# Performance work log

Measured on AMD Instinct MI355X. Metric: run time of the kernel, lower is better.

Reference implementation:

```python
import jax, jax.numpy as jnp
import numpy as np

H = 150
PASSES = 5
NSETS = 2
N = 50000
E = 400000
G = 64
SLOPE = 0.01  # torch leaky_relu default


def setup_inputs() -> dict:
    key = jax.random.key(0)
    ks = jax.random.split(key, 20)
    def u(k, shape, fan):
        lim = 1.0 / np.sqrt(fan)
        return jax.random.uniform(k, shape, jnp.float32, -lim, lim)
    return {
        "nodes": jax.random.normal(ks[0], (N, H), jnp.float32),
        "problem_type": jax.random.uniform(ks[1], (G, 1), jnp.float32),
        "edge_W": u(ks[2], (NSETS, H, H), H),
        "edge_b": u(ks[3], (NSETS, H), H),
        "gru_w_ih": u(ks[4], (3 * H, H), H),
        "gru_w_hh": u(ks[5], (3 * H, H), H),
        "gru_b_ih": u(ks[6], (3 * H,), H),
        "gru_b_hh": u(ks[7], (3 * H,), H),
        "fc1_w": u(ks[8], (80, 151), 151),
        "fc1_b": u(ks[9], (80,), 151),
        "fc2_w": u(ks[10], (80, 80), 80),
        "fc2_b": u(ks[11], (80,), 80),
        "fcL_w": u(ks[12], (10, 80), 80),
        "fcL_b": u(ks[13], (10,), 80),
        "edges": jax.random.randint(ks[14], (NSETS, E, 2), 0, N),
        "graph_ids": jnp.sort(jax.random.randint(ks[15], (N,), 0, G)),
        "tbptt": 0,
    }


def _gru_cell(x, h, w_ih, w_hh, b_ih, b_hh):
    gi = x @ w_ih.T + b_ih  # [N, 3H]
    gh = h @ w_hh.T + b_hh
    ir, iz, inn = jnp.split(gi, 3, axis=-1)
    hr, hz, hn = jnp.split(gh, 3, axis=-1)
    r = jax.nn.sigmoid(ir + hr)
    z = jax.nn.sigmoid(iz + hz)
    n = jnp.tanh(inn + r * hn)
    return (1.0 - z) * n + z * h


def reference(nodes, problem_type, edge_W, edge_b, gru_w_ih, gru_w_hh,
              gru_b_ih, gru_b_hh, fc1_w, fc1_b, fc2_w, fc2_b, fcL_w, fcL_b,
              edges, graph_ids, tbptt):
    n_sets = edge_W.shape[0]
    n_graphs = problem_type.shape[0]
    for j in range(PASSES):
        incoming = jnp.zeros_like(nodes)
        for k in range(n_sets):
            src = edges[k, :, 1]
            dst = edges[k, :, 0]
            # NOTE: in the source, the first Linear+leaky_relu result is
            # overwritten; the effective edge message is just the second Linear.
            y = nodes[src] @ edge_W[k].T + edge_b[k]  # [E, H]
            incoming = incoming.at[dst].add(y)
        nodes = _gru_cell(incoming, nodes, gru_w_ih, gru_w_hh, gru_b_ih, gru_b_hh)
        if tbptt == 1 and j < PASSES - 2:
            nodes = jax.lax.stop_gradient(nodes)
    g = jax.ops.segment_sum(nodes, graph_ids, num_segments=n_graphs)  # [G, H]
    g = jnp.log(g)
    g = jnp.where(jnp.isnan(g), 0.0, g)
    g = jax.nn.relu(g)
    x = jnp.concatenate([g, problem_type], axis=1)  # [G, 151]
    x = jax.nn.leaky_relu(x @ fc1_w.T + fc1_b, SLOPE)
    x = jax.nn.leaky_relu(x @ fc2_w.T + fc2_b, SLOPE)
    return x @ fcL_w.T + fcL_b  # [G, 10]
```

## Files before the change

### kernel.cpp

```cpp
#include <hip/hip_runtime.h>
#include <stdint.h>

#define NN 50000
#define H 150
#define NE 400000
#define NG 64
#define NPASS 5
#define KB 480
#define VC 640
#define NRB 391

typedef unsigned short u16;
typedef unsigned int u32;
typedef __attribute__((ext_vector_type(8))) short short8;
typedef __attribute__((ext_vector_type(4))) float float4v;
typedef __attribute__((ext_vector_type(4))) u32 uint4v;

__device__ __forceinline__ u16 f2bf_rn(float x) {
  union { float f; u32 u; } v; v.f = x;
  u32 r = v.u + 0x7fffu + ((v.u >> 16) & 1u);
  return (u16)(r >> 16);
}
__device__ __forceinline__ float bf2f(u16 h) {
  union { u32 u; float f; } v; v.u = ((u32)h) << 16;
  return v.f;
}
__device__ __forceinline__ u32 packf(float v) {
  u16 hi = f2bf_rn(v);
  u16 lo = f2bf_rn(v - bf2f(hi));
  return (u32)hi | ((u32)lo << 16);
}
__device__ __forceinline__ float upk(u32 u) {
  union { u32 u; float f; } a, b;
  a.u = u << 16; b.u = u & 0xffff0000u;
  return a.f + b.f;
}
__device__ __forceinline__ void async16(const void* g, void* l) {
  __builtin_amdgcn_global_load_lds(
      (const __attribute__((address_space(1))) unsigned int*)(uintptr_t)g,
      (__attribute__((address_space(3))) unsigned int*)(uint32_t)(uintptr_t)l,
      16, 0, 0);
}

__global__ void hist_kernel(const int* __restrict__ edges, int* __restrict__ cnt) {
  int id = blockIdx.x * 256 + threadIdx.x;
  if (id >= 2 * NE) return;
  int dst = edges[id * 2];
  int set = id / NE;
  atomicAdd(&cnt[dst * 2 + set], 1);
}

__global__ __launch_bounds__(1024) void scan1_kernel(const int* __restrict__ cnt,
                                                     int* __restrict__ rowptr,
                                                     int* __restrict__ bsum, int n) {
  __shared__ int sd[1024];
  int t = threadIdx.x;
  int idx = blockIdx.x * 1024 + t;
  int v = (idx < n) ? cnt[idx] : 0;
  sd[t] = v;
  __syncthreads();
  for (int off = 1; off < 1024; off <<= 1) {
    int add = (t >= off) ? sd[t - off] : 0;
    __syncthreads();
    sd[t] += add;
    __syncthreads();
  }
  if (idx < n) rowptr[idx] = sd[t] - v;
  if (t == 1023) bsum[blockIdx.x] = sd[1023];
}

__global__ __launch_bounds__(128) void scan2_kernel(const int* __restrict__ bsum,
                                                    int* __restrict__ boff, int nb) {
  __shared__ int sd[128];
  int t = threadIdx.x;
  int v = (t < nb) ? bsum[t] : 0;
  sd[t] = v;
  __syncthreads();
  for (int off = 1; off < 128; off <<= 1) {
    int add = (t >= off) ? sd[t - off] : 0;
    __syncthreads();
    sd[t] += add;
    __syncthreads();
  }
  boff[t] = sd[t] - v;
}

__global__ void scan3_kernel(int* __restrict__ rowptr, const int* __restrict__ boff,
                             int n, int nb) {
  int idx = blockIdx.x * 256 + threadIdx.x;
  if (idx < n) rowptr[idx] += boff[idx >> 10];
  if (idx == 0) rowptr[n] = boff[nb];
}

__global__ void copy_int_kernel(const int* __restrict__ a, int* __restrict__ b, int n) {
  int id = blockIdx.x * 256 + threadIdx.x;
  if (id < n) b[id] = a[id];
}

__global__ void fill_kernel(const int* __restrict__ edges, int* __restrict__ cursor,
                            u16* __restrict__ colbuf) {
  int id = blockIdx.x * 256 + threadIdx.x;
  if (id >= 2 * NE) return;
  int dst = edges[id * 2];
  int src = edges[id * 2 + 1];
  int set = id / NE;
  int pos = atomicAdd(&cursor[dst * 2 + set], 1);
  colbuf[pos] = (u16)src;
}

__global__ void bounds_kernel(const int* __restrict__ gids, int* __restrict__ gstart) {
  int g = threadIdx.x;
  if (g > NG) return;
  int lo = 0, hi = NN;
  while (lo < hi) { int m = (lo + hi) >> 1; if (gids[m] < g) lo = m + 1; else hi = m; }
  gstart[g] = lo;
}

__global__ void build_B_kernel(const float* __restrict__ wih, const float* __restrict__ whh,
                               const float* __restrict__ eW,
                               u16* __restrict__ Bh, u16* __restrict__ Bl) {
  int id = blockIdx.x * 256 + threadIdx.x;
  if (id >= VC * KB) return;
  int v = id / KB, k = id % KB;
  int g = (v >> 4) & 3, c = (v >> 6) * 16 + (v & 15);
  int seg = k / 160, kk = k % 160;
  float val = 0.f;
  if (c < H && kk < H) {
    if (seg < 2) {
      if (g < 3) {
        const float* wr = wih + (size_t)(g * H + c) * H;
        const float* wc = eW + (size_t)seg * H * H + kk;
        float acc = 0.f;
        for (int t = 0; t < H; t++) acc += wr[t] * wc[(size_t)t * H];
        val = acc;
      }
    } else {
      if (g == 0) val = whh[(size_t)c * H + kk];
      else if (g == 1) val = whh[(size_t)(H + c) * H + kk];
      else if (g == 3) val = whh[(size_t)(2 * H + c) * H + kk];
    }
  }
  u16 h = f2bf_rn(val);
  Bh[id] = h;
  Bl[id] = f2bf_rn(val - bf2f(h));
}

__global__ void build_coef_kernel(const float* __restrict__ wih,
                                  const float* __restrict__ eb,
                                  const float* __restrict__ bih, const float* __restrict__ bhh,
                                  float* __restrict__ coefs) {
  int id = threadIdx.x + blockIdx.x * 256;
  if (id >= VC) return;
  int g = id / 160, c = id % 160;
  float u0 = 0.f, u1 = 0.f, bs = 0.f;
  if (c < H) {
    if (g < 3) {
      const float* wr = wih + (size_t)(g * H + c) * H;
      for (int t = 0; t < H; t++) { u0 += wr[t] * eb[t]; u1 += wr[t] * eb[H + t]; }
    }
    if (g == 0) bs = bih[c] + bhh[c];
    else if (g == 1) bs = bih[H + c] + bhh[H + c];
    else if (g == 2) bs = bih[2 * H + c];
    else bs = bhh[2 * H + c];
  }
  coefs[id] = u0;
  coefs[VC + id] = u1;
  coefs[2 * VC + id] = bs;
}

__global__ void init_nodes_kernel(const float* __restrict__ nin,
                                  u32* __restrict__ npkA, u32* __restrict__ npkB) {
  int id = blockIdx.x * 256 + threadIdx.x;
  if (id >= NN * 40) return;
  int r = id / 40, q = id % 40;
  int c = q * 4;
  uint4v a;
  const float* src = nin + (size_t)r * H + c;
  u32 w0 = 0, w1 = 0, w2 = 0, w3 = 0;
  if (c + 3 < H) {
    w0 = packf(src[0]); w1 = packf(src[1]); w2 = packf(src[2]); w3 = packf(src[3]);
  } else {
    if (c < H) w0 = packf(src[0]);
    if (c + 1 < H) w1 = packf(src[1]);
    if (c + 2 < H) w2 = packf(src[2]);
  }
  a.x = w0; a.y = w1; a.z = w2; a.w = w3;
  *(uint4v*)(npkA + (size_t)r * 160 + c) = a;
  if (c >= 148) {
    uint4v z = {0, 0, 0, 0};
    if (c >= 152) *(uint4v*)(npkB + (size_t)r * 160 + c) = z;
    else if (c == 148) { npkB[(size_t)r * 160 + 150] = 0; npkB[(size_t)r * 160 + 151] = 0; }
  }
}

__global__ void pad_S_kernel(u32* __restrict__ Snp) {
  int id = blockIdx.x * 256 + threadIdx.x;
  if (id >= NN * 20) return;
  int r = id / 20, rem = id % 20;
  int set = rem / 10, t = rem % 10;
  Snp[(size_t)r * 320 + set * 160 + H + t] = 0;
}

__global__ __launch_bounds__(256) void gather_kernel(
    const u32* __restrict__ npk, const int* __restrict__ rowptr,
    const u16* __restrict__ colbuf, u32* __restrict__ Snp) {
  int gtid = blockIdx.x * 256 + threadIdx.x;
  int wid = gtid >> 6;
  if (wid >= 2 * NN) return;
  int node = wid >> 1, set = wid & 1;
  int lane = gtid & 63;
  int s = rowptr[2 * node + set], e = rowptr[2 * node + set + 1];
  int deg = e - s;
  int c4 = 4 * lane;
  bool ok = (lane < 40);
  float a0 = 0.f, a1 = 0.f, a2 = 0.f, a3 = 0.f;
  for (int base = 0; base < deg; base += 64) {
    int rem = min(64, deg - base);
    u32 srcv = 0;
    if (lane < rem) srcv = (u32)colbuf[s + base + lane];
    int i = 0;
    for (; i + 3 < rem; i += 4) {
      int r0 = __builtin_amdgcn_readlane((int)srcv, i);
      int r1 = __builtin_amdgcn_readlane((int)srcv, i + 1);
      int r2 = __builtin_amdgcn_readlane((int)srcv, i + 2);
      int r3 = __builtin_amdgcn_readlane((int)srcv, i + 3);
      uint4v v0 = {0, 0, 0, 0}, v1 = {0, 0, 0, 0};
      uint4v v2 = {0, 0, 0, 0}, v3 = {0, 0, 0, 0};
      if (ok) {
        v0 = *(const uint4v*)(npk + (size_t)(u32)r0 * 160 + c4);
        v1 = *(const uint4v*)(npk + (size_t)(u32)r1 * 160 + c4);
        v2 = *(const uint4v*)(npk + (size_t)(u32)r2 * 160 + c4);
        v3 = *(const uint4v*)(npk + (size_t)(u32)r3 * 160 + c4);
      }
      a0 += upk(v0.x) + upk(v1.x);
      a1 += upk(v0.y) + upk(v1.y);
      a2 += upk(v0.z) + upk(v1.z);
      a3 += upk(v0.w) + upk(v1.w);
      a0 += upk(v2.x) + upk(v3.x);
      a1 += upk(v2.y) + upk(v3.y);
      a2 += upk(v2.z) + upk(v3.z);
      a3 += upk(v2.w) + upk(v3.w);
    }
    for (; i + 1 < rem; i += 2) {
      int r0 = __builtin_amdgcn_readlane((int)srcv, i);
      int r1 = __builtin_amdgcn_readlane((int)srcv, i + 1);
      uint4v v0 = {0, 0, 0, 0}, v1 = {0, 0, 0, 0};
      if (ok) {
        v0 = *(const uint4v*)(npk + (size_t)(u32)r0 * 160 + c4);
        v1 = *(const uint4v*)(npk + (size_t)(u32)r1 * 160 + c4);
      }
      a0 += upk(v0.x) + upk(v1.x);
      a1 += upk(v0.y) + upk(v1.y);
      a2 += upk(v0.z) + upk(v1.z);
      a3 += upk(v0.w) + upk(v1.w);
    }
    if (i < rem) {
      int r0 = __builtin_amdgcn_readlane((int)srcv, i);
      uint4v v0 = {0, 0, 0, 0};
      if (ok) v0 = *(const uint4v*)(npk + (size_t)(u32)r0 * 160 + c4);
      a0 += upk(v0.x);
      a1 += upk(v0.y);
      a2 += upk(v0.z);
      a3 += upk(v0.w);
    }
  }
  if (ok) {
    uint4v pv;
    pv.x = packf(a0);
    pv.y = packf(a1);
    pv.z = packf(a2);
    pv.w = packf(a3);
    *(uint4v*)(Snp + (size_t)node * 320 + set * 160 + c4) = pv;
  }
}


template<int KT>
__device__ __forceinline__ void stage_fn(
    const u32* __restrict__ Snp, const u32* __restrict__ npkc,
    const u16* __restrict__ Bhp, const u16* __restrict__ Blp,
    char* Ab, char* Bb, int tid, int w, int r0, int ccb) {
  #pragma unroll
  for (int i = 0; i < 4; i++) {
    int cl = i * 256 + tid;
    int row = cl >> 3;
    int q = (cl & 7) ^ (row & 7);
    int rg = min(r0 + row, NN - 1);
    if constexpr (KT < 10)
      async16(Snp + (size_t)rg * 320 + KT * 32 + q * 4, Ab + i * 4096 + w * 1024);
    else
      async16(npkc + (size_t)rg * 160 + (KT - 10) * 32 + q * 4, Ab + i * 4096 + w * 1024);
  }
  constexpr int koffB = (KT < 10) ? KT * 32 : 320 + (KT - 10) * 32;
  constexpr int skipg = (KT < 10) ? 3 : 2;
  #pragma unroll
  for (int i = 0; i < 2; i++) {
    int cl = i * 256 + tid;
    int row = cl >> 2;
    int q = (cl & 3) ^ ((row >> 1) & 3);
    if (((row >> 4) & 3) != skipg) {
      size_t gb = (size_t)(ccb * 128 + row) * KB + koffB + q * 8;
      int lb = i * 4096 + w * 1024;
      async16(Bhp + gb, Bb + lb);
      async16(Blp + gb, Bb + 8192 + lb);
    }
  }
}

template<int KTn>
__device__ __forceinline__ void read_frags_fn(
    const char* Ab, const char* Bb, int m, int quad, int mrow0, int nco0,
    uint4v (&A0)[4], uint4v (&A1)[4], short8 (&RBh)[3], short8 (&RBl)[3]) {
  #pragma unroll
  for (int jj = 0; jj < 3; jj++) {
    const int jsel = (jj == 2) ? ((KTn < 10) ? 2 : 3) : jj;
    int br = nco0 + jsel * 16 + m;
    int bd = br * 64 + ((quad ^ ((br >> 1) & 3)) * 16);
    RBh[jj] = *(const short8*)(Bb + bd);
    RBl[jj] = *(const short8*)(Bb + 8192 + bd);
  }
  #pragma unroll
  for (int mt = 0; mt < 4; mt++) {
    int r = mrow0 + mt * 16 + m;
    A0[mt] = *(const uint4v*)(Ab + r * 128 + (((2 * quad) ^ (r & 7)) * 16));
    A1[mt] = *(const uint4v*)(Ab + r * 128 + (((2 * quad + 1) ^ (r & 7)) * 16));
  }
}

template<int KT>
__device__ __forceinline__ void mfma_fn(
    const uint4v (&A0)[4], const uint4v (&A1)[4],
    const short8 (&MBh)[3], const short8 (&MBl)[3], float4v (&acc)[4][4]) {
  #pragma unroll
  for (int mt = 0; mt < 4; mt++) {
    u32 uu[8] = {A0[mt].x, A0[mt].y, A0[mt].z, A0[mt].w,
                 A1[mt].x, A1[mt].y, A1[mt].z, A1[mt].w};
    short8 ah, al;
    #pragma unroll
    for (int e2 = 0; e2 < 8; e2++) {
      ah[e2] = (short)(uu[e2] & 0xffffu);
      al[e2] = (short)(uu[e2] >> 16);
    }
    #pragma unroll
    for (int jj = 0; jj < 3; jj++) {
      const int J = (KT < 10) ? jj : ((jj == 2) ? 3 : jj);
      acc[mt][J] = __builtin_amdgcn_mfma_f32_16x16x32_bf16(ah, MBh[jj], acc[mt][J], 0, 0, 0);
      acc[mt][J] = __builtin_amdgcn_mfma_f32_16x16x32_bf16(ah, MBl[jj], acc[mt][J], 0, 0, 0);
      acc[mt][J] = __builtin_amdgcn_mfma_f32_16x16x32_bf16(al, MBh[jj], acc[mt][J], 0, 0, 0);
    }
  }
}

template<int K0>
__device__ __forceinline__ void gemm_superstep(
    const u32* __restrict__ Snp, const u32* __restrict__ npkc,
    const u16* __restrict__ Bhp, const u16* __restrict__ Blp,
    char (&Abuf)[2][16384], char (&Bbuf)[2][16384],
    int tid, int w, int m, int quad, int mrow0, int nco0, int r0, int ccb,
    float4v (&acc)[4][4]) {
  constexpr int K1 = K0 + 1;
  uint4v A0a[4], A1a[4], A0b[4], A1b[4];
  short8 FBha[3], FBla[3], FBhb[3], FBlb[3];
  read_frags_fn<K0>(Abuf[0], Bbuf[0], m, quad, mrow0, nco0, A0a, A1a, FBha, FBla);
  if constexpr (K1 <= 14)
    read_frags_fn<K1>(Abuf[1], Bbuf[1], m, quad, mrow0, nco0, A0b, A1b, FBhb, FBlb);
  asm volatile("s_waitcnt lgkmcnt(0)" ::: "memory");
  __builtin_amdgcn_sched_barrier(0);
  if constexpr (K0 + 2 <= 14) {
    __builtin_amdgcn_s_barrier();
    stage_fn<K0 + 2>(Snp, npkc, Bhp, Blp, Abuf[0], Bbuf[0], tid, w, r0, ccb);
    if constexpr (K1 + 2 <= 14)
      stage_fn<K1 + 2>(Snp, npkc, Bhp, Blp, Abuf[1], Bbuf[1], tid, w, r0, ccb);
    __builtin_amdgcn_sched_barrier(0);
  }
  __builtin_amdgcn_s_setprio(1);
  mfma_fn<K0>(A0a, A1a, FBha, FBla, acc);
  if constexpr (K1 <= 14)
    mfma_fn<K1>(A0b, A1b, FBhb, FBlb, acc);
  __builtin_amdgcn_s_setprio(0);
  __builtin_amdgcn_sched_barrier(0);
  if constexpr (K0 + 2 <= 14) {
    asm volatile("s_waitcnt vmcnt(0)" ::: "memory");
    __builtin_amdgcn_sched_barrier(0);
    __builtin_amdgcn_s_barrier();
  }
}

__global__ __launch_bounds__(256, 2) void gru_gemm_kernel(
    const u32* __restrict__ Snp, const u32* __restrict__ npkc,
    const u16* __restrict__ Bhp, const u16* __restrict__ Blp,
    const float* __restrict__ coefs, const int* __restrict__ rowptr,
    u32* __restrict__ npkn) {
  __shared__ char Abuf[2][16384];
  __shared__ char Bbuf[2][16384];
  const int bid = blockIdx.x;
  const int xcd = bid & 7;
  const int rest = bid >> 3;
  const int ccb = rest % 5;
  const int r0b = (rest / 5) * 8 + xcd;
  if (r0b >= NRB) return;
  const int r0 = r0b * 128;
  const int tid = threadIdx.x;
  const int w = tid >> 6, l = tid & 63;
  const int m = l & 15, quad = l >> 4;
  const int mrow0 = (w & 1) * 64;
  const int nco0 = (w >> 1) * 64;

  float4v acc[4][4];
  #pragma unroll
  for (int mt = 0; mt < 4; mt++)
    #pragma unroll
    for (int j = 0; j < 4; j++) acc[mt][j] = (float4v){0.f, 0.f, 0.f, 0.f};

  stage_fn<0>(Snp, npkc, Bhp, Blp, Abuf[0], Bbuf[0], tid, w, r0, ccb);
  stage_fn<1>(Snp, npkc, Bhp, Blp, Abuf[1], Bbuf[1], tid, w, r0, ccb);
  asm volatile("s_waitcnt vmcnt(0)" ::: "memory");
  __builtin_amdgcn_sched_barrier(0);
  __builtin_amdgcn_s_barrier();

  #define SSTEP(K) gemm_superstep<K>(Snp, npkc, Bhp, Blp, Abuf, Bbuf, tid, w, m, \
                                     quad, mrow0, nco0, r0, ccb, acc)
  SSTEP(0); SSTEP(2); SSTEP(4); SSTEP(6);
  SSTEP(8); SSTEP(10); SSTEP(12); SSTEP(14);
  #undef SSTEP

  int c = (ccb * 2 + (w >> 1)) * 16 + m;
  if (c >= H) return;
  float u0r = coefs[c],            u0z = coefs[160 + c],
        u0n = coefs[320 + c];
  float u1r = coefs[VC + c],       u1z = coefs[VC + 160 + c],
        u1n = coefs[VC + 320 + c];
  float bsr = coefs[2 * VC + c],   bsz = coefs[2 * VC + 160 + c],
        bsn = coefs[2 * VC + 320 + c], bsh = coefs[2 * VC + 480 + c];
  #pragma unroll
  for (int mt = 0; mt < 4; mt++) {
    #pragma unroll
    for (int i = 0; i < 4; i++) {
      int row = r0 + mrow0 + mt * 16 + quad * 4 + i;
      if (row >= NN) continue;
      float d0 = (float)(rowptr[2 * row + 1] - rowptr[2 * row]);
      float d1 = (float)(rowptr[2 * row + 2] - rowptr[2 * row + 1]);
      float pr = acc[mt][0][i] + d0 * u0r + d1 * u1r + bsr;
      float pz = acc[mt][1][i] + d0 * u0z + d1 * u1z + bsz;
      float pn = acc[mt][2][i] + d0 * u0n + d1 * u1n + bsn;
      float ph = acc[mt][3][i] + bsh;
      float r_g = 1.f / (1.f + __expf(-pr));
      float z_g = 1.f / (1.f + __expf(-pz));
      float narg = pn + r_g * ph;
      float e2 = __expf(2.f * narg);
      float n_g = 1.f - 2.f / (e2 + 1.f);
      float h = upk(npkc[(size_t)row * 160 + c]);
      npkn[(size_t)row * 160 + c] = packf((1.f - z_g) * n_g + z_g * h);
    }
  }
}

__global__ __launch_bounds__(192) void segsum_kernel(const u32* __restrict__ npk,
                                                     const int* __restrict__ gstart,
                                                     float* __restrict__ gsum) {
  int g = blockIdx.x, chunk = blockIdx.y;
  int c = threadIdx.x;
  if (c >= H) return;
  int s = gstart[g], e = gstart[g + 1];
  int len = e - s;
  if (len <= 0) return;
  int per = (len + 15) / 16;
  int rs = s + chunk * per;
  int re = min(e, rs + per);
  if (rs >= re) return;
  float acc = 0.f;
  for (int r = rs; r < re; r++) acc += upk(npk[(size_t)r * 160 + c]);
  atomicAdd(&gsum[g * H + c], acc);
}

__global__ __launch_bounds__(192) void head_kernel(
    const float* __restrict__ gsum, const float* __restrict__ pt,
    const float* __restrict__ fc1_w, const float* __restrict__ fc1_b,
    const float* __restrict__ fc2_w, const float* __restrict__ fc2_b,
    const float* __restrict__ fcL_w, const float* __restrict__ fcL_b,
    float* __restrict__ out) {
  __shared__ float x[151];
  __shared__ float x1[80];
  __shared__ float x2[80];
  int row = blockIdx.x;
  int t = threadIdx.x;
  if (t < 151) {
    float v;
    if (t < H) { float g = gsum[row * H + t]; v = (g > 1.f) ? logf(g) : 0.f; }
    else v = pt[row];
    x[t] = v;
  }
  __syncthreads();
  if (t < 80) {
    float acc = fc1_b[t];
    const float* wrow = fc1_w + t * 151;
    #pragma unroll 4
    for (int k = 0; k < 151; k++) acc += x[k] * wrow[k];
    x1[t] = (acc > 0.f) ? acc : 0.01f * acc;
  }
  __syncthreads();
  if (t < 80) {
    float acc = fc2_b[t];
    const float* wrow = fc2_w + t * 80;
    #pragma unroll 4
    for (int k = 0; k < 80; k++) acc += x1[k] * wrow[k];
    x2[t] = (acc > 0.f) ? acc : 0.01f * acc;
  }
  __syncthreads();
  if (t < 10) {
    float acc = fcL_b[t];
    const float* wrow = fcL_w + t * 80;
    #pragma unroll 4
    for (int k = 0; k < 80; k++) acc += x2[k] * wrow[k];
    out[row * 10 + t] = acc;
  }
}

extern "C" void kernel_launch(void* const* d_in, const int* in_sizes, int n_in,
                              void* d_out, int out_size, void* d_ws, size_t ws_size,
                              hipStream_t stream) {
  const float* nodes_in = (const float*)d_in[0];
  const float* problem_type = (const float*)d_in[1];
  const float* edge_W = (const float*)d_in[2];
  const float* edge_b = (const float*)d_in[3];
  const float* w_ih = (const float*)d_in[4];
  const float* w_hh = (const float*)d_in[5];
  const float* b_ih = (const float*)d_in[6];
  const float* b_hh = (const float*)d_in[7];
  const float* fc1_w = (const float*)d_in[8];
  const float* fc1_b = (const float*)d_in[9];
  const float* fc2_w = (const float*)d_in[10];
  const float* fc2_b = (const float*)d_in[11];
  const float* fcL_w = (const float*)d_in[12];
  const float* fcL_b = (const float*)d_in[13];
  const int* edges = (const int*)d_in[14];
  const int* graph_ids = (const int*)d_in[15];

  char* ws = (char*)d_ws;
  size_t off = 0;
  auto alloc = [&](size_t bytes) -> void* {
    void* p = ws + off;
    off = (off + bytes + 255) & ~(size_t)255;
    return p;
  };
  u32* npkA     = (u32*)alloc((size_t)NN * 160 * 4);
  u32* npkB     = (u32*)alloc((size_t)NN * 160 * 4);
  u32* Snp      = (u32*)alloc((size_t)NN * 320 * 4);
  u16* Bh       = (u16*)alloc((size_t)VC * KB * 2);
  u16* Bl       = (u16*)alloc((size_t)VC * KB * 2);
  float* coefs  = (float*)alloc(3 * VC * 4);
  int* rowptr   = (int*)alloc((2 * NN + 1) * 4);
  int* cursor   = (int*)alloc(2 * NN * 4);
  u16* colbuf   = (u16*)alloc(2ull * NE * 2);
  int* bsum     = (int*)alloc(128 * 4);
  int* boff     = (int*)alloc(128 * 4);
  int* gstart   = (int*)alloc((NG + 1) * 4);
  float* gsum   = (float*)alloc((size_t)NG * H * 4);

  const int n2 = 2 * NN;
  const int nb = (n2 + 1023) / 1024;

  hipMemsetAsync(cursor, 0, n2 * 4, stream);
  hist_kernel<<<(2 * NE + 255) / 256, 256, 0, stream>>>(edges, cursor);
  scan1_kernel<<<nb, 1024, 0, stream>>>(cursor, rowptr, bsum, n2);
  scan2_kernel<<<1, 128, 0, stream>>>(bsum, boff, nb);
  scan3_kernel<<<(n2 + 255) / 256, 256, 0, stream>>>(rowptr, boff, n2, nb);
  copy_int_kernel<<<(n2 + 255) / 256, 256, 0, stream>>>(rowptr, cursor, n2);
  fill_kernel<<<(2 * NE + 255) / 256, 256, 0, stream>>>(edges, cursor, colbuf);
  bounds_kernel<<<1, 128, 0, stream>>>(graph_ids, gstart);
  build_B_kernel<<<(VC * KB + 255) / 256, 256, 0, stream>>>(w_ih, w_hh, edge_W, Bh, Bl);
  build_coef_kernel<<<(VC + 255) / 256, 256, 0, stream>>>(w_ih, edge_b, b_ih, b_hh, coefs);
  init_nodes_kernel<<<(NN * 40 + 255) / 256, 256, 0, stream>>>(nodes_in, npkA, npkB);
  pad_S_kernel<<<(NN * 20 + 255) / 256, 256, 0, stream>>>(Snp);

  const int ngrp = (NRB + 7) / 8;
  u32* nbuf[2] = {npkA, npkB};
  for (int pass = 0; pass < NPASS; pass++) {
    u32* cur = nbuf[pass & 1];
    u32* nxt = nbuf[1 - (pass & 1)];
    gather_kernel<<<(2 * NN * 64 + 255) / 256, 256, 0, stream>>>(cur, rowptr, colbuf, Snp);
    gru_gemm_kernel<<<ngrp * 5 * 8, 256, 0, stream>>>(
        Snp, cur, Bh, Bl, coefs, rowptr, nxt);
  }
  u32* fin = nbuf[NPASS & 1];

  hipMemsetAsync(gsum, 0, (size_t)NG * H * 4, stream);
  segsum_kernel<<<dim3(NG, 16), 192, 0, stream>>>(fin, gstart, gsum);
  head_kernel<<<NG, 192, 0, stream>>>(gsum, problem_type, fc1_w, fc1_b, fc2_w, fc2_b,
                                      fcL_w, fcL_b, (float*)d_out);
}
```

Measured before the change: 1.107 ms.

## Restructure GRU GEMM so each block covers all output columns for 64 rows

The GRU GEMM now uses 512-thread blocks. Each block handles 64 node rows and loops over all five column blocks, instead of launching one block per 128x128 tile. A-operand tiles (aggregated messages plus current node state) are staged once per group of three k-tiles and reused across every column block, which removes repeated global reads of A. B tiles are streamed double-buffered with a barrier after every k-tile, so per-step MFMA work is small and synchronisation is frequent. The separate padding kernel for the aggregation buffer is dropped, since the gather kernel already writes the padded columns.

```diff
diff --git a/kernel.cpp b/kernel.cpp
--- a/kernel.cpp
+++ b/kernel.cpp
@@ -8,7 +8,8 @@
 #define NPASS 5
 #define KB 480
 #define VC 640
-#define NRB 391
+#define RPB 64
+#define NBLK ((NN + RPB - 1) / RPB)
 
 typedef unsigned short u16;
 typedef unsigned int u32;
@@ -191,14 +192,6 @@
     if (c >= 152) *(uint4v*)(npkB + (size_t)r * 160 + c) = z;
     else if (c == 148) { npkB[(size_t)r * 160 + 150] = 0; npkB[(size_t)r * 160 + 151] = 0; }
   }
-}
-
-__global__ void pad_S_kernel(u32* __restrict__ Snp) {
-  int id = blockIdx.x * 256 + threadIdx.x;
-  if (id >= NN * 20) return;
-  int r = id / 20, rem = id % 20;
-  int set = rem / 10, t = rem % 10;
-  Snp[(size_t)r * 320 + set * 160 + H + t] = 0;
 }
 
 __global__ __launch_bounds__(256) void gather_kernel(
@@ -274,176 +267,160 @@
   }
 }
 
-
-template<int KT>
-__device__ __forceinline__ void stage_fn(
-    const u32* __restrict__ Snp, const u32* __restrict__ npkc,
-    const u16* __restrict__ Bhp, const u16* __restrict__ Blp,
-    char* Ab, char* Bb, int tid, int w, int r0, int ccb) {
-  #pragma unroll
-  for (int i = 0; i < 4; i++) {
-    int cl = i * 256 + tid;
-    int row = cl >> 3;
-    int q = (cl & 7) ^ (row & 7);
-    int rg = min(r0 + row, NN - 1);
-    if constexpr (KT < 10)
-      async16(Snp + (size_t)rg * 320 + KT * 32 + q * 4, Ab + i * 4096 + w * 1024);
-    else
-      async16(npkc + (size_t)rg * 160 + (KT - 10) * 32 + q * 4, Ab + i * 4096 + w * 1024);
-  }
-  constexpr int koffB = (KT < 10) ? KT * 32 : 320 + (KT - 10) * 32;
-  constexpr int skipg = (KT < 10) ? 3 : 2;
-  #pragma unroll
-  for (int i = 0; i < 2; i++) {
-    int cl = i * 256 + tid;
-    int row = cl >> 2;
-    int q = (cl & 3) ^ ((row >> 1) & 3);
-    if (((row >> 4) & 3) != skipg) {
-      size_t gb = (size_t)(ccb * 128 + row) * KB + koffB + q * 8;
-      int lb = i * 4096 + w * 1024;
-      async16(Bhp + gb, Bb + lb);
-      async16(Blp + gb, Bb + 8192 + lb);
-    }
-  }
-}
-
-template<int KTn>
-__device__ __forceinline__ void read_frags_fn(
-    const char* Ab, const char* Bb, int m, int quad, int mrow0, int nco0,
-    uint4v (&A0)[4], uint4v (&A1)[4], short8 (&RBh)[3], short8 (&RBl)[3]) {
-  #pragma unroll
-  for (int jj = 0; jj < 3; jj++) {
-    const int jsel = (jj == 2) ? ((KTn < 10) ? 2 : 3) : jj;
-    int br = nco0 + jsel * 16 + m;
-    int bd = br * 64 + ((quad ^ ((br >> 1) & 3)) * 16);
-    RBh[jj] = *(const short8*)(Bb + bd);
-    RBl[jj] = *(const short8*)(Bb + 8192 + bd);
-  }
-  #pragma unroll
-  for (int mt = 0; mt < 4; mt++) {
-    int r = mrow0 + mt * 16 + m;
-    A0[mt] = *(const uint4v*)(Ab + r * 128 + (((2 * quad) ^ (r & 7)) * 16));
-    A1[mt] = *(const uint4v*)(Ab + r * 128 + (((2 * quad + 1) ^ (r & 7)) * 16));
-  }
-}
-
-template<int KT>
-__device__ __forceinline__ void mfma_fn(
-    const uint4v (&A0)[4], const uint4v (&A1)[4],
-    const short8 (&MBh)[3], const short8 (&MBl)[3], float4v (&acc)[4][4]) {
-  #pragma unroll
-  for (int mt = 0; mt < 4; mt++) {
-    u32 uu[8] = {A0[mt].x, A0[mt].y, A0[mt].z, A0[mt].w,
-                 A1[mt].x, A1[mt].y, A1[mt].z, A1[mt].w};
-    short8 ah, al;
-    #pragma unroll
-    for (int e2 = 0; e2 < 8; e2++) {
-      ah[e2] = (short)(uu[e2] & 0xffffu);
-      al[e2] = (short)(uu[e2] >> 16);
-    }
-    #pragma unroll
-    for (int jj = 0; jj < 3; jj++) {
-      const int J = (KT < 10) ? jj : ((jj == 2) ? 3 : jj);
-      acc[mt][J] = __builtin_amdgcn_mfma_f32_16x16x32_bf16(ah, MBh[jj], acc[mt][J], 0, 0, 0);
-      acc[mt][J] = __builtin_amdgcn_mfma_f32_16x16x32_bf16(ah, MBl[jj], acc[mt][J], 0, 0, 0);
-      acc[mt][J] = __builtin_amdgcn_mfma_f32_16x16x32_bf16(al, MBh[jj], acc[mt][J], 0, 0, 0);
-    }
-  }
-}
-
-template<int K0>
-__device__ __forceinline__ void gemm_superstep(
-    const u32* __restrict__ Snp, const u32* __restrict__ npkc,
-    const u16* __restrict__ Bhp, const u16* __restrict__ Blp,
-    char (&Abuf)[2][16384], char (&Bbuf)[2][16384],
-    int tid, int w, int m, int quad, int mrow0, int nco0, int r0, int ccb,
-    float4v (&acc)[4][4]) {
-  constexpr int K1 = K0 + 1;
-  uint4v A0a[4], A1a[4], A0b[4], A1b[4];
-  short8 FBha[3], FBla[3], FBhb[3], FBlb[3];
-  read_frags_fn<K0>(Abuf[0], Bbuf[0], m, quad, mrow0, nco0, A0a, A1a, FBha, FBla);
-  if constexpr (K1 <= 14)
-    read_frags_fn<K1>(Abuf[1], Bbuf[1], m, quad, mrow0, nco0, A0b, A1b, FBhb, FBlb);
-  asm volatile("s_waitcnt lgkmcnt(0)" ::: "memory");
-  __builtin_amdgcn_sched_barrier(0);
-  if constexpr (K0 + 2 <= 14) {
-    __builtin_amdgcn_s_barrier();
-    stage_fn<K0 + 2>(Snp, npkc, Bhp, Blp, Abuf[0], Bbuf[0], tid, w, r0, ccb);
-    if constexpr (K1 + 2 <= 14)
-      stage_fn<K1 + 2>(Snp, npkc, Bhp, Blp, Abuf[1], Bbuf[1], tid, w, r0, ccb);
-    __builtin_amdgcn_sched_barrier(0);
-  }
-  __builtin_amdgcn_s_setprio(1);
-  mfma_fn<K0>(A0a, A1a, FBha, FBla, acc);
-  if constexpr (K1 <= 14)
-    mfma_fn<K1>(A0b, A1b, FBhb, FBlb, acc);
-  __builtin_amdgcn_s_setprio(0);
-  __builtin_amdgcn_sched_barrier(0);
-  if constexpr (K0 + 2 <= 14) {
-    asm volatile("s_waitcnt vmcnt(0)" ::: "memory");
-    __builtin_amdgcn_sched_barrier(0);
-    __builtin_amdgcn_s_barrier();
-  }
-}
-
-__global__ __launch_bounds__(256, 2) void gru_gemm_kernel(
+__global__ __launch_bounds__(512, 2) void gru_gemm_kernel(
     const u32* __restrict__ Snp, const u32* __restrict__ npkc,
     const u16* __restrict__ Bhp, const u16* __restrict__ Blp,
     const float* __restrict__ coefs, const int* __restrict__ rowptr,
     u32* __restrict__ npkn) {
-  __shared__ char Abuf[2][16384];
+  __shared__ char Abuf[24576];
   __shared__ char Bbuf[2][16384];
-  const int bid = blockIdx.x;
-  const int xcd = bid & 7;
-  const int rest = bid >> 3;
-  const int ccb = rest % 5;
-  const int r0b = (rest / 5) * 8 + xcd;
-  if (r0b >= NRB) return;
-  const int r0 = r0b * 128;
+  const int r0 = blockIdx.x * RPB;
   const int tid = threadIdx.x;
   const int w = tid >> 6, l = tid & 63;
   const int m = l & 15, quad = l >> 4;
-  const int mrow0 = (w & 1) * 64;
-  const int nco0 = (w >> 1) * 64;
-
-  float4v acc[4][4];
+  const int wm = w & 3, wn = w >> 2;
+
+  float4v acc[5][4];
   #pragma unroll
-  for (int mt = 0; mt < 4; mt++)
+  for (int cc = 0; cc < 5; cc++)
     #pragma unroll
-    for (int j = 0; j < 4; j++) acc[mt][j] = (float4v){0.f, 0.f, 0.f, 0.f};
-
-  stage_fn<0>(Snp, npkc, Bhp, Blp, Abuf[0], Bbuf[0], tid, w, r0, ccb);
-  stage_fn<1>(Snp, npkc, Bhp, Blp, Abuf[1], Bbuf[1], tid, w, r0, ccb);
+    for (int j = 0; j < 4; j++) acc[cc][j] = (float4v){0.f, 0.f, 0.f, 0.f};
+
+  auto stageA = [&](int kq) {
+    #pragma unroll
+    for (int i = 0; i < 3; i++) {
+      int cl = i * 512 + tid;
+      int row = cl / 24;
+      int rem = cl - row * 24;
+      int ktl = rem >> 3;
+      int q = (rem & 7) ^ (row & 7);
+      int kt = kq * 3 + ktl;
+      int rg = min(r0 + row, NN - 1);
+      const u32* src = (kt < 10)
+          ? (Snp + (size_t)rg * 320 + kt * 32 + q * 4)
+          : (npkc + (size_t)rg * 160 + (kt - 10) * 32 + q * 4);
+      async16(src, Abuf + i * 8192 + w * 1024);
+    }
+  };
+  auto stageB = [&](int ccbn, int ktn, char* Bb) {
+    int row = tid >> 2;
+    int q = (tid & 3) ^ ((row >> 1) & 3);
+    int skipg = (ktn < 10) ? 3 : 2;
+    int koffB = (ktn < 10) ? ktn * 32 : 320 + (ktn - 10) * 32;
+    if (((row >> 4) & 3) != skipg) {
+      size_t gb = (size_t)(ccbn * 128 + row) * KB + koffB + q * 8;
+      async16(Bhp + gb, Bb + w * 1024);
+      async16(Blp + gb, Bb + 8192 + w * 1024);
+    }
+  };
+
+  stageA(0);
+  stageB(0, 0, Bbuf[0]);
   asm volatile("s_waitcnt vmcnt(0)" ::: "memory");
   __builtin_amdgcn_sched_barrier(0);
   __builtin_amdgcn_s_barrier();
 
-  #define SSTEP(K) gemm_superstep<K>(Snp, npkc, Bhp, Blp, Abuf, Bbuf, tid, w, m, \
-                                     quad, mrow0, nco0, r0, ccb, acc)
-  SSTEP(0); SSTEP(2); SSTEP(4); SSTEP(6);
-  SSTEP(8); SSTEP(10); SSTEP(12); SSTEP(14);
-  #undef SSTEP
-
-  int c = (ccb * 2 + (w >> 1)) * 16 + m;
-  if (c >= H) return;
-  float u0r = coefs[c],            u0z = coefs[160 + c],
-        u0n = coefs[320 + c];
-  float u1r = coefs[VC + c],       u1z = coefs[VC + 160 + c],
-        u1n = coefs[VC + 320 + c];
-  float bsr = coefs[2 * VC + c],   bsz = coefs[2 * VC + 160 + c],
-        bsn = coefs[2 * VC + 320 + c], bsh = coefs[2 * VC + 480 + c];
+  #pragma unroll 1
+  for (int kq = 0; kq < 5; kq++) {
+    #pragma unroll
+    for (int ccb = 0; ccb < 5; ccb++) {
+      #pragma unroll
+      for (int ktl = 0; ktl < 3; ktl++) {
+        const int kt = kq * 3 + ktl;
+        const int par = (kq + ccb + ktl) & 1;
+        char* Bb = Bbuf[par];
+        char* Bn = Bbuf[par ^ 1];
+        const bool lo10 = (kt < 10);
+        short8 bh[3], bl[3];
+        #pragma unroll
+        for (int jj = 0; jj < 3; jj++) {
+          int jsel = (jj == 2) ? (lo10 ? 2 : 3) : jj;
+          int br = wn * 64 + jsel * 16 + m;
+          int bd = br * 64 + ((quad ^ ((br >> 1) & 3)) * 16);
+          bh[jj] = *(const short8*)(Bb + bd);
+          bl[jj] = *(const short8*)(Bb + 8192 + bd);
+        }
+        int r = wm * 16 + m;
+        int abase = r * 384 + ktl * 128;
+        uint4v A0 = *(const uint4v*)(Abuf + abase + (((2 * quad) ^ (r & 7)) * 16));
+        uint4v A1 = *(const uint4v*)(Abuf + abase + (((2 * quad + 1) ^ (r & 7)) * 16));
+        asm volatile("s_waitcnt lgkmcnt(0)" ::: "memory");
+        __builtin_amdgcn_sched_barrier(0);
+        {
+          int nktl = ktl + 1, nccb = ccb, nkq = kq;
+          if (nktl == 3) { nktl = 0; nccb++; }
+          if (nccb == 5) { nccb = 0; nkq++; }
+          if (nkq < 5) stageB(nccb, nkq * 3 + nktl, Bn);
+        }
+        if (ccb == 4 && ktl == 2) {
+          __builtin_amdgcn_s_barrier();
+          if (kq < 4) stageA(kq + 1);
+        }
+        __builtin_amdgcn_sched_barrier(0);
+        u32 uu[8] = {A0.x, A0.y, A0.z, A0.w, A1.x, A1.y, A1.z, A1.w};
+        short8 ah, al;
+        #pragma unroll
+        for (int e2 = 0; e2 < 8; e2++) {
+          ah[e2] = (short)(uu[e2] & 0xffffu);
+          al[e2] = (short)(uu[e2] >> 16);
+        }
+        __builtin_amdgcn_s_setprio(1);
+        if (lo10) {
+          #pragma unroll
+          for (int jj = 0; jj < 3; jj++) {
+            acc[ccb][jj] = __builtin_amdgcn_mfma_f32_16x16x32_bf16(ah, bh[jj], acc[ccb][jj], 0, 0, 0);
+            acc[ccb][jj] = __builtin_amdgcn_mfma_f32_16x16x32_bf16(ah, bl[jj], acc[ccb][jj], 0, 0, 0);
+            acc[ccb][jj] = __builtin_amdgcn_mfma_f32_16x16x32_bf16(al, bh[jj], acc[ccb][jj], 0, 0, 0);
+          }
+        } else {
+          acc[ccb][0] = __builtin_amdgcn_mfma_f32_16x16x32_bf16(ah, bh[0], acc[ccb][0], 0, 0, 0);
+          acc[ccb][0] = __builtin_amdgcn_mfma_f32_16x16x32_bf16(ah, bl[0], acc[ccb][0], 0, 0, 0);
+          acc[ccb][0] = __builtin_amdgcn_mfma_f32_16x16x32_bf16(al, bh[0], acc[ccb][0], 0, 0, 0);
+          acc[ccb][1] = __builtin_amdgcn_mfma_f32_16x16x32_bf16(ah, bh[1], acc[ccb][1], 0, 0, 0);
+          acc[ccb][1] = __builtin_amdgcn_mfma_f32_16x16x32_bf16(ah, bl[1], acc[ccb][1], 0, 0, 0);
+          acc[ccb][1] = __builtin_amdgcn_mfma_f32_16x16x32_bf16(al, bh[1], acc[ccb][1], 0, 0, 0);
+          acc[ccb][3] = __builtin_amdgcn_mfma_f32_16x16x32_bf16(ah, bh[2], acc[ccb][3], 0, 0, 0);
+          acc[ccb][3] = __builtin_amdgcn_mfma_f32_16x16x32_bf16(ah, bl[2], acc[ccb][3], 0, 0, 0);
+          acc[ccb][3] = __builtin_amdgcn_mfma_f32_16x16x32_bf16(al, bh[2], acc[ccb][3], 0, 0, 0);
+        }
+        __builtin_amdgcn_s_setprio(0);
+        __builtin_amdgcn_sched_barrier(0);
+        asm volatile("s_waitcnt vmcnt(0)" ::: "memory");
+        __builtin_amdgcn_sched_barrier(0);
+        __builtin_amdgcn_s_barrier();
+      }
+    }
+  }
+
+  int rows[4];
+  float d0v[4], d1v[4];
   #pragma unroll
-  for (int mt = 0; mt < 4; mt++) {
+  for (int i = 0; i < 4; i++) {
+    int row = r0 + wm * 16 + quad * 4 + i;
+    rows[i] = row;
+    if (row < NN) {
+      d0v[i] = (float)(rowptr[2 * row + 1] - rowptr[2 * row]);
+      d1v[i] = (float)(rowptr[2 * row + 2] - rowptr[2 * row + 1]);
+    } else { d0v[i] = 0.f; d1v[i] = 0.f; }
+  }
+  #pragma unroll
+  for (int ccb = 0; ccb < 5; ccb++) {
+    int c = (ccb * 2 + wn) * 16 + m;
+    if (c >= H) continue;
+    float u0r = coefs[c],            u0z = coefs[160 + c],
+          u0n = coefs[320 + c];
+    float u1r = coefs[VC + c],       u1z = coefs[VC + 160 + c],
+          u1n = coefs[VC + 320 + c];
+    float bsr = coefs[2 * VC + c],   bsz = coefs[2 * VC + 160 + c],
+          bsn = coefs[2 * VC + 320 + c], bsh = coefs[2 * VC + 480 + c];
     #pragma unroll
     for (int i = 0; i < 4; i++) {
-      int row = r0 + mrow0 + mt * 16 + quad * 4 + i;
+      int row = rows[i];
       if (row >= NN) continue;
-      float d0 = (float)(rowptr[2 * row + 1] - rowptr[2 * row]);
-      float d1 = (float)(rowptr[2 * row + 2] - rowptr[2 * row + 1]);
-      float pr = acc[mt][0][i] + d0 * u0r + d1 * u1r + bsr;
-      float pz = acc[mt][1][i] + d0 * u0z + d1 * u1z + bsz;
-      float pn = acc[mt][2][i] + d0 * u0n + d1 * u1n + bsn;
-      float ph = acc[mt][3][i] + bsh;
+      float pr = acc[ccb][0][i] + d0v[i] * u0r + d1v[i] * u1r + bsr;
+      float pz = acc[ccb][1][i] + d0v[i] * u0z + d1v[i] * u1z + bsz;
+      float pn = acc[ccb][2][i] + d0v[i] * u0n + d1v[i] * u1n + bsn;
+      float ph = acc[ccb][3][i] + bsh;
       float r_g = 1.f / (1.f + __expf(-pr));
       float z_g = 1.f / (1.f + __expf(-pz));
       float narg = pn + r_g * ph;
@@ -571,15 +548,13 @@
   build_B_kernel<<<(VC * KB + 255) / 256, 256, 0, stream>>>(w_ih, w_hh, edge_W, Bh, Bl);
   build_coef_kernel<<<(VC + 255) / 256, 256, 0, stream>>>(w_ih, edge_b, b_ih, b_hh, coefs);
   init_nodes_kernel<<<(NN * 40 + 255) / 256, 256, 0, stream>>>(nodes_in, npkA, npkB);
-  pad_S_kernel<<<(NN * 20 + 255) / 256, 256, 0, stream>>>(Snp);
-
-  const int ngrp = (NRB + 7) / 8;
+
   u32* nbuf[2] = {npkA, npkB};
   for (int pass = 0; pass < NPASS; pass++) {
     u32* cur = nbuf[pass & 1];
     u32* nxt = nbuf[1 - (pass & 1)];
     gather_kernel<<<(2 * NN * 64 + 255) / 256, 256, 0, stream>>>(cur, rowptr, colbuf, Snp);
-    gru_gemm_kernel<<<ngrp * 5 * 8, 256, 0, stream>>>(
+    gru_gemm_kernel<<<NBLK, 512, 0, stream>>>(
         Snp, cur, Bh, Bl, coefs, rowptr, nxt);
   }
   u32* fin = nbuf[NPASS & 1];
```

New measurement: 1.723 ms. 1.56x slower.
